# Kernel tuning notes

Measured on AMD Instinct MI355X. Metric: run time of the kernel, lower is better.

## Reference

```python
import jax, jax.numpy as jnp
from jax import lax
import numpy as np

B, T, I, H = 256, 1024, 128, 256


def setup_inputs() -> dict:
    key = jax.random.key(0)
    k1, k2, k3 = jax.random.split(key, 3)
    # Xavier-ish scaling so sigmoid/tanh gates are not saturated
    s_ih = float(np.sqrt(2.0 / (I + 3 * H)))
    s_hh = float(np.sqrt(2.0 / (H + 3 * H)))
    return {
        "x": jax.random.normal(k1, (B, T, I), dtype=jnp.float32),
        "h0": jnp.zeros((B, H), dtype=jnp.float32),
        "weight_ih": jax.random.normal(k2, (3 * H, I), dtype=jnp.float32) * s_ih,
        "weight_hh": jax.random.normal(k3, (3 * H, H), dtype=jnp.float32) * s_hh,
        "bias_ih": jnp.zeros((3 * H,), dtype=jnp.float32),
        "bias_hh": jnp.zeros((3 * H,), dtype=jnp.float32),
    }


def reference(x, h0, weight_ih, weight_hh, bias_ih, bias_hh):
    # Precompute batched input-to-hidden GEMM for all timesteps: [B, T, 3H]
    gates_x = jnp.einsum("bti,gi->btg", x, weight_ih) + bias_ih
    gates_x = jnp.swapaxes(gates_x, 0, 1)  # [T, B, 3H] for scan

    def step(h, gx):
        # NOTE: faithful to source — reset gate multiplies the FULL new-gate
        # preactivation (which already includes the hidden contribution),
        # unlike a standard GRU.
        gates = gx + h @ weight_hh.T + bias_hh  # [B, 3H]
        r, z, n = jnp.split(gates, 3, axis=-1)
        r = jax.nn.sigmoid(r)
        z = jax.nn.sigmoid(z)
        n = jnp.tanh(r * n)
        h_new = (1.0 - z) * h + z * n
        return h_new, h_new

    h_last, outs = lax.scan(step, h0, gates_x)  # outs: [T, B, H]
    output = jnp.swapaxes(outs, 0, 1)  # [B, T, H] (batch_first=True)
    return output, h_last
```

## Files before the change

### kernel.cpp

```cpp
#include <hip/hip_runtime.h>


#define B_SZ 256
#define T_SZ 1024
#define H_SZ 256
#define G3   768
#define NGRP 64
#define SPIN_MAX (1 << 21)
#define HROW 288

typedef __attribute__((ext_vector_type(2))) float f32x2;

template<int CTRL>
__device__ __forceinline__ float dppx(float s) {
    return __int_as_float(
        __builtin_amdgcn_update_dpp(0, __float_as_int(s), CTRL, 0xF, 0xF, true));
}
template<int MASK>
__device__ __forceinline__ float swzx(float s) {
    return __int_as_float(__builtin_amdgcn_ds_swizzle(__float_as_int(s), MASK));
}
__device__ __forceinline__ f32x2 pkfma(f32x2 a, f32x2 b, f32x2 c) {
    f32x2 d;
    asm("v_pk_fma_f32 %0, %1, %2, %3" : "=v"(d) : "v"(a), "v"(b), "v"(c));
    return d;
}

static __device__ __forceinline__ int hpos(int k) { return k + 4 * (k >> 5); }

static __device__ __forceinline__ size_t xsl(int g, int par, int n, int u) {
    return (((size_t)g * 2 + par) * 4 + n) * 256 + u;
}

__global__ void prep_kernel(const float* __restrict__ h0,
                            unsigned long long* __restrict__ xch) {
    int tid = blockIdx.x * blockDim.x + threadIdx.x;
    if (tid < B_SZ * H_SZ) {
        int b = tid >> 8, u = tid & 255;
        int g = b >> 2, n = b & 3;
        unsigned long long val = (unsigned long long)__float_as_uint(h0[tid]);
        xch[xsl(g, 0, n, u)] = val;
        xch[xsl(g, 1, n, u)] = val;
    }
}

__global__ __launch_bounds__(256) void gemm_x_kernel(
    const float* __restrict__ x, const float* __restrict__ wih,
    float* __restrict__ gx, int c, int tcShift)
{
    __shared__ __align__(16) float xs[64][132];
    __shared__ __align__(16) float ws[128][68];
    const int TC = 1 << tcShift;
    const int t  = threadIdx.x;
    const int bx = blockIdx.x, by = blockIdx.y;

#pragma unroll
    for (int i = 0; i < 8; ++i) {
        int f4 = t + i * 256;
        int r  = f4 >> 5, c4 = (f4 & 31) * 4;
        int rho = bx * 64 + r;
        int b = rho >> tcShift, u = rho & (TC - 1);
        float4 v = *(const float4*)(x + ((size_t)b * T_SZ + (size_t)c * TC + u) * 128 + c4);
        *(float4*)&xs[r][c4] = v;
    }

    const int gl = t & 31;
    const int rl = t >> 5;
    float acc[8][4];
#pragma unroll
    for (int i = 0; i < 8; ++i)
#pragma unroll
        for (int jj = 0; jj < 4; ++jj) acc[i][jj] = 0.f;

    for (int kb = 0; kb < 2; ++kb) {
        __syncthreads();
#pragma unroll
        for (int i = 0; i < 8; ++i) {
            int f4 = t + i * 256;
            int row = f4 >> 4, c4 = (f4 & 15) * 4;
            float4 v = *(const float4*)(wih + (size_t)(by * 128 + row) * 128 + kb * 64 + c4);
            *(float4*)&ws[row][c4] = v;
        }
        __syncthreads();

#pragma unroll 4
        for (int k4 = 0; k4 < 16; ++k4) {
            float4 wv0 = *(const float4*)&ws[gl     ][k4 * 4];
            float4 wv1 = *(const float4*)&ws[gl + 32][k4 * 4];
            float4 wv2 = *(const float4*)&ws[gl + 64][k4 * 4];
            float4 wv3 = *(const float4*)&ws[gl + 96][k4 * 4];
#pragma unroll
            for (int rr = 0; rr < 8; ++rr) {
                float4 xv = *(const float4*)&xs[rl + rr * 8][kb * 64 + k4 * 4];
                acc[rr][0] = fmaf(xv.w, wv0.w, fmaf(xv.z, wv0.z, fmaf(xv.y, wv0.y, fmaf(xv.x, wv0.x, acc[rr][0]))));
                acc[rr][1] = fmaf(xv.w, wv1.w, fmaf(xv.z, wv1.z, fmaf(xv.y, wv1.y, fmaf(xv.x, wv1.x, acc[rr][1]))));
                acc[rr][2] = fmaf(xv.w, wv2.w, fmaf(xv.z, wv2.z, fmaf(xv.y, wv2.y, fmaf(xv.x, wv2.x, acc[rr][2]))));
                acc[rr][3] = fmaf(xv.w, wv3.w, fmaf(xv.z, wv3.z, fmaf(xv.y, wv3.y, fmaf(xv.x, wv3.x, acc[rr][3]))));
            }
        }
    }

#pragma unroll
    for (int rr = 0; rr < 8; ++rr) {
        size_t base = (size_t)(bx * 64 + rl + rr * 8) * G3 + by * 128 + gl;
#pragma unroll
        for (int gi = 0; gi < 4; ++gi)
            gx[base + 32 * gi] = acc[rr][gi];
    }
}

#define PIN2(v) asm volatile("" : "+v"(v));

__global__ __launch_bounds__(512)
__attribute__((amdgpu_waves_per_eu(2, 2)))
void gru_kernel(
    const float* __restrict__ gx, const float* __restrict__ whh,
    const float* __restrict__ bih, const float* __restrict__ bhh,
    unsigned long long* __restrict__ xch, float* __restrict__ out,
    int gbase, int tc, int isLast)
{
    __shared__ __align__(16) float hl[2][4][HROW];
    __shared__ __align__(16) float hst[2][4][64];

    const int t   = threadIdx.x;
    const int bid = blockIdx.x;
    const int g   = bid & 63;
    const int m   = bid >> 6;
    const int u0  = m * 64;
    const int q   = t >> 5;
    const int p   = t & 31;
    const int pb  = p & 3;
    const int uq  = u0 + 4 * q;
    const int k0  = 8 * p;

    f32x2 wf[12][4];
#pragma unroll
    for (int gate = 0; gate < 3; ++gate) {
#pragma unroll
        for (int e = 0; e < 4; ++e) {
            const float* wr = whh + (size_t)(gate * 256 + uq + e) * H_SZ + k0;
            float4 va = *(const float4*)(wr);
            float4 vb = *(const float4*)(wr + 4);
            wf[gate * 4 + e][0] = (f32x2){va.x, va.y};
            wf[gate * 4 + e][1] = (f32x2){va.z, va.w};
            wf[gate * 4 + e][2] = (f32x2){vb.x, vb.y};
            wf[gate * 4 + e][3] = (f32x2){vb.z, vb.w};
        }
    }
#pragma unroll
    for (int f = 0; f < 12; ++f) {
        PIN2(wf[f][0]) PIN2(wf[f][1]) PIN2(wf[f][2]) PIN2(wf[f][3])
    }

    const bool act = (p < 16);
    const int  e   = (p >> 2) & 3;
    const int  ue  = uq + e;
    float bsr = 0.f, bsz = 0.f, bsn = 0.f;
    const float* gxp = nullptr;
    if (act) {
        bsr = bih[ue]       + bhh[ue];
        bsz = bih[256 + ue] + bhh[256 + ue];
        bsn = bih[512 + ue] + bhh[512 + ue];
        gxp = gx + ((size_t)(4 * g + pb) * tc) * G3 + ue;
    }

    const int n_t  = t >> 7;
    const int c2   = t & 127;
    const int wofs = 2 * c2 + 4 * (c2 >> 4);
    const int Wd = hpos(k0);
    const int pue = hpos(ue);
    const int n_o = t >> 4, f_o = t & 15;

    float gxr = 0.f, gxz = 0.f, gxn = 0.f;
    if (act) { gxr = gxp[0]; gxz = gxp[256]; gxn = gxp[512]; }

#pragma unroll 1
    for (int u = 0; u < tc; ++u) {
        const int tg   = gbase + u;
        const int par  = tg & 1;
        const int par1 = (tg + 1) & 1;

        {
            unsigned long long* sb = xch + xsl(g, par, n_t, 2 * c2);
            const unsigned want = (unsigned)tg;
            unsigned long long v0, v1;
            int sp = 0;
            for (;;) {
                v0 = __hip_atomic_load(sb + 0, __ATOMIC_RELAXED, __HIP_MEMORY_SCOPE_AGENT);
                v1 = __hip_atomic_load(sb + 1, __ATOMIC_RELAXED, __HIP_MEMORY_SCOPE_AGENT);
                bool ok = ((unsigned)(v0 >> 32) == want) & ((unsigned)(v1 >> 32) == want);
                if (ok || ++sp >= SPIN_MAX) break;
                __builtin_amdgcn_s_sleep(1);
            }
            float2 hv;
            hv.x = __uint_as_float((unsigned)v0);
            hv.y = __uint_as_float((unsigned)v1);
            *(float2*)&hl[par][n_t][wofs] = hv;
        }
        __syncthreads();

        if (u > 0 && t < 64) {
            float4 o;
            o.x = hst[par1][n_o][4 * f_o];     o.y = hst[par1][n_o][4 * f_o + 1];
            o.z = hst[par1][n_o][4 * f_o + 2]; o.w = hst[par1][n_o][4 * f_o + 3];
            *(float4*)(out + ((size_t)(4 * g + n_o) * T_SZ + (tg - 1)) * H_SZ + u0 + 4 * f_o) = o;
        }

        float pgr = 0.f, pgz = 0.f, pgn = 0.f;
        if (act && u + 1 < tc) {
            size_t go = (size_t)(u + 1) * G3;
            pgr = gxp[go]; pgz = gxp[go + 256]; pgn = gxp[go + 512];
        }

        float s[12][4];
        {
            const float* hb = &hl[par][0][0] + Wd;
#pragma unroll
            for (int i = 0; i < 4; ++i) {
                const float* hr = hb + (size_t)(i ^ pb) * HROW;
                float4 hv0 = *(const float4*)(hr);
                float4 hv1 = *(const float4*)(hr + 4);
                f32x2 h0 = (f32x2){hv0.x, hv0.y};
                f32x2 h1 = (f32x2){hv0.z, hv0.w};
                f32x2 h2 = (f32x2){hv1.x, hv1.y};
                f32x2 h3 = (f32x2){hv1.z, hv1.w};
                f32x2 z  = (f32x2){0.f, 0.f};
#pragma unroll
                for (int f = 0; f < 12; ++f) {
                    f32x2 a = pkfma(h0, wf[f][0],
                              pkfma(h1, wf[f][1],
                              pkfma(h2, wf[f][2],
                              pkfma(h3, wf[f][3], z))));
                    s[f][i] = a.x + a.y;
                }
            }
        }

#pragma unroll
        for (int f = 0; f < 12; ++f) {
            s[f][0] += dppx<0xB1>(s[f][1]);
            s[f][2] += dppx<0xB1>(s[f][3]);
            s[f][0] += dppx<0x4E>(s[f][2]);
            s[f][0] += dppx<0x124>(s[f][0]);
            s[f][0] += dppx<0x128>(s[f][0]);
            s[f][0] += swzx<0x401F>(s[f][0]);
        }

        if (act) {
            float sr = (e & 2) ? ((e & 1) ? s[3][0]  : s[2][0])
                               : ((e & 1) ? s[1][0]  : s[0][0]);
            float sz = (e & 2) ? ((e & 1) ? s[7][0]  : s[6][0])
                               : ((e & 1) ? s[5][0]  : s[4][0]);
            float sn = (e & 2) ? ((e & 1) ? s[11][0] : s[10][0])
                               : ((e & 1) ? s[9][0]  : s[8][0]);

            float hold = hl[par][pb][pue];
            float ar = sr + gxr + bsr;
            float az = sz + gxz + bsz;
            float an = sn + gxn + bsn;
            float r  = 1.f / (1.f + expf(-ar));
            float z  = 1.f / (1.f + expf(-az));
            float nn = tanhf(r * an);
            float hn = (1.f - z) * hold + z * nn;

            hst[par][pb][ue - u0] = hn;
            __hip_atomic_store(xch + xsl(g, par1, pb, ue),
                               ((unsigned long long)(unsigned)(tg + 1) << 32) |
                               (unsigned long long)__float_as_uint(hn),
                               __ATOMIC_RELAXED, __HIP_MEMORY_SCOPE_AGENT);
        }
        gxr = pgr; gxz = pgz; gxn = pgn;
    }

    __syncthreads();
    {
        const int fpar = (gbase + tc - 1) & 1;
        if (t < 64) {
            float4 o;
            o.x = hst[fpar][n_o][4 * f_o];     o.y = hst[fpar][n_o][4 * f_o + 1];
            o.z = hst[fpar][n_o][4 * f_o + 2]; o.w = hst[fpar][n_o][4 * f_o + 3];
            *(float4*)(out + ((size_t)(4 * g + n_o) * T_SZ + (gbase + tc - 1)) * H_SZ + u0 + 4 * f_o) = o;
            if (isLast)
                *(float4*)(out + (size_t)B_SZ * T_SZ * H_SZ
                               + (size_t)(4 * g + n_o) * H_SZ + u0 + 4 * f_o) = o;
        }
    }
}

extern "C" void kernel_launch(void* const* d_in, const int* in_sizes, int n_in,
                              void* d_out, int out_size, void* d_ws, size_t ws_size,
                              hipStream_t stream) {
    const float* x   = (const float*)d_in[0];
    const float* h0  = (const float*)d_in[1];
    const float* wih = (const float*)d_in[2];
    const float* whh = (const float*)d_in[3];
    const float* bih = (const float*)d_in[4];
    const float* bhh = (const float*)d_in[5];
    float* out = (float*)d_out;

    char* ws = (char*)d_ws;
    const size_t xchB = (size_t)NGRP * 2 * 4 * 256 * 8;
    unsigned long long* xch = (unsigned long long*)ws;
    float* gxb = (float*)(ws + xchB);

    int tcShift = 10;
    while (tcShift > 0 &&
           xchB + (786432ull << tcShift) > ws_size) --tcShift;
    const int TC  = 1 << tcShift;
    const int nCh = T_SZ / TC;

    prep_kernel<<<dim3(256), dim3(256), 0, stream>>>(h0, xch);
    for (int c = 0; c < nCh; ++c) {
        gemm_x_kernel<<<dim3(B_SZ * TC / 64, 6), dim3(256), 0, stream>>>(
            x, wih, gxb, c, tcShift);
        gru_kernel<<<dim3(B_SZ), dim3(512), 0, stream>>>(
            gxb, whh, bih, bhh, xch, out, c * TC, TC, (c == nCh - 1) ? 1 : 0);
    }
}
```

Baseline: 3.712 ms.

## Repartition GRU blocks to 2 batch rows by 128 hidden units each

Each recurrent block now handles 2 batch rows and 128 hidden units instead of 4 rows and 64 units, so 128 groups cover the batch. Each thread keeps twice as many recurrent weight rows in registers (24 packed rows), and the cross-lane reduction drops one shuffle stage. The intent is to cut the number of rows each block must gather through the global exchange buffer and to shorten the reduction chain per step. In exchange, register pressure roughly doubles for weights, and a second barrier is added per timestep, with hst reused across steps without parity.

Result: slower. 5.913 ms (+59.3%).

```diff
diff --git a/kernel.cpp b/kernel.cpp
--- a/kernel.cpp
+++ b/kernel.cpp
@@ -5,7 +5,7 @@
 #define T_SZ 1024
 #define H_SZ 256
 #define G3   768
-#define NGRP 64
+#define NGRP 128
 #define SPIN_MAX (1 << 21)
 #define HROW 288
 
@@ -29,7 +29,7 @@
 static __device__ __forceinline__ int hpos(int k) { return k + 4 * (k >> 5); }
 
 static __device__ __forceinline__ size_t xsl(int g, int par, int n, int u) {
-    return (((size_t)g * 2 + par) * 4 + n) * 256 + u;
+    return (((size_t)g * 2 + par) * 2 + n) * 256 + u;
 }
 
 __global__ void prep_kernel(const float* __restrict__ h0,
@@ -37,7 +37,7 @@
     int tid = blockIdx.x * blockDim.x + threadIdx.x;
     if (tid < B_SZ * H_SZ) {
         int b = tid >> 8, u = tid & 255;
-        int g = b >> 2, n = b & 3;
+        int g = b >> 1, n = b & 1;
         unsigned long long val = (unsigned long long)__float_as_uint(h0[tid]);
         xch[xsl(g, 0, n, u)] = val;
         xch[xsl(g, 1, n, u)] = val;
@@ -119,92 +119,85 @@
     unsigned long long* __restrict__ xch, float* __restrict__ out,
     int gbase, int tc, int isLast)
 {
-    __shared__ __align__(16) float hl[2][4][HROW];
-    __shared__ __align__(16) float hst[2][4][64];
+    __shared__ __align__(16) float hl[2][HROW];
+    __shared__ __align__(16) float hst[2][128];
 
     const int t   = threadIdx.x;
     const int bid = blockIdx.x;
-    const int g   = bid & 63;
-    const int m   = bid >> 6;
-    const int u0  = m * 64;
+    const int g   = bid & 127;
+    const int m   = bid >> 7;
+    const int u0  = m * 128;
     const int q   = t >> 5;
     const int p   = t & 31;
-    const int pb  = p & 3;
-    const int uq  = u0 + 4 * q;
+    const int pb  = p & 1;
+    const int uo  = u0 + 8 * q;
     const int k0  = 8 * p;
 
-    f32x2 wf[12][4];
+    f32x2 wf[24][4];
 #pragma unroll
     for (int gate = 0; gate < 3; ++gate) {
 #pragma unroll
-        for (int e = 0; e < 4; ++e) {
-            const float* wr = whh + (size_t)(gate * 256 + uq + e) * H_SZ + k0;
+        for (int e = 0; e < 8; ++e) {
+            const float* wr = whh + (size_t)(gate * 256 + uo + e) * H_SZ + k0;
             float4 va = *(const float4*)(wr);
             float4 vb = *(const float4*)(wr + 4);
-            wf[gate * 4 + e][0] = (f32x2){va.x, va.y};
-            wf[gate * 4 + e][1] = (f32x2){va.z, va.w};
-            wf[gate * 4 + e][2] = (f32x2){vb.x, vb.y};
-            wf[gate * 4 + e][3] = (f32x2){vb.z, vb.w};
-        }
-    }
-#pragma unroll
-    for (int f = 0; f < 12; ++f) {
+            wf[gate * 8 + e][0] = (f32x2){va.x, va.y};
+            wf[gate * 8 + e][1] = (f32x2){va.z, va.w};
+            wf[gate * 8 + e][2] = (f32x2){vb.x, vb.y};
+            wf[gate * 8 + e][3] = (f32x2){vb.z, vb.w};
+        }
+    }
+#pragma unroll
+    for (int f = 0; f < 24; ++f) {
         PIN2(wf[f][0]) PIN2(wf[f][1]) PIN2(wf[f][2]) PIN2(wf[f][3])
     }
 
     const bool act = (p < 16);
-    const int  e   = (p >> 2) & 3;
-    const int  ue  = uq + e;
+    const int  e   = p >> 1;
+    const int  ue  = uo + e;
     float bsr = 0.f, bsz = 0.f, bsn = 0.f;
     const float* gxp = nullptr;
     if (act) {
         bsr = bih[ue]       + bhh[ue];
         bsz = bih[256 + ue] + bhh[256 + ue];
         bsn = bih[512 + ue] + bhh[512 + ue];
-        gxp = gx + ((size_t)(4 * g + pb) * tc) * G3 + ue;
-    }
-
-    const int n_t  = t >> 7;
-    const int c2   = t & 127;
-    const int wofs = 2 * c2 + 4 * (c2 >> 4);
-    const int Wd = hpos(k0);
-    const int pue = hpos(ue);
-    const int n_o = t >> 4, f_o = t & 15;
+        gxp = gx + ((size_t)(2 * g + pb) * tc) * G3 + ue;
+    }
+
+    const int n_t  = t >> 8;
+    const int un   = t & 255;
+    const int wofs = hpos(un);
+    const int Wd   = hpos(k0);
+    const int pue  = hpos(ue);
+    const int n_o = t >> 5, f_o = t & 31;
 
     float gxr = 0.f, gxz = 0.f, gxn = 0.f;
     if (act) { gxr = gxp[0]; gxz = gxp[256]; gxn = gxp[512]; }
 
 #pragma unroll 1
     for (int u = 0; u < tc; ++u) {
-        const int tg   = gbase + u;
-        const int par  = tg & 1;
-        const int par1 = (tg + 1) & 1;
-
-        {
-            unsigned long long* sb = xch + xsl(g, par, n_t, 2 * c2);
-            const unsigned want = (unsigned)tg;
-            unsigned long long v0, v1;
-            int sp = 0;
-            for (;;) {
-                v0 = __hip_atomic_load(sb + 0, __ATOMIC_RELAXED, __HIP_MEMORY_SCOPE_AGENT);
-                v1 = __hip_atomic_load(sb + 1, __ATOMIC_RELAXED, __HIP_MEMORY_SCOPE_AGENT);
-                bool ok = ((unsigned)(v0 >> 32) == want) & ((unsigned)(v1 >> 32) == want);
-                if (ok || ++sp >= SPIN_MAX) break;
-                __builtin_amdgcn_s_sleep(1);
-            }
-            float2 hv;
-            hv.x = __uint_as_float((unsigned)v0);
-            hv.y = __uint_as_float((unsigned)v1);
-            *(float2*)&hl[par][n_t][wofs] = hv;
-        }
-        __syncthreads();
+        const int tg  = gbase + u;
+        const int par = tg & 1;
 
         if (u > 0 && t < 64) {
             float4 o;
-            o.x = hst[par1][n_o][4 * f_o];     o.y = hst[par1][n_o][4 * f_o + 1];
-            o.z = hst[par1][n_o][4 * f_o + 2]; o.w = hst[par1][n_o][4 * f_o + 3];
-            *(float4*)(out + ((size_t)(4 * g + n_o) * T_SZ + (tg - 1)) * H_SZ + u0 + 4 * f_o) = o;
-        }
+            o.x = hst[n_o][4 * f_o];     o.y = hst[n_o][4 * f_o + 1];
+            o.z = hst[n_o][4 * f_o + 2]; o.w = hst[n_o][4 * f_o + 3];
+            *(float4*)(out + ((size_t)(2 * g + n_o) * T_SZ + (tg - 1)) * H_SZ + u0 + 4 * f_o) = o;
+        }
+
+        {
+            unsigned long long* sb = xch + xsl(g, par, n_t, un);
+            const unsigned want = (unsigned)tg;
+            unsigned long long v = __hip_atomic_load(sb, __ATOMIC_RELAXED, __HIP_MEMORY_SCOPE_AGENT);
+            int sp = 0;
+            while ((unsigned)(v >> 32) != want && ++sp < SPIN_MAX) {
+                __builtin_amdgcn_s_sleep(1);
+                v = __hip_atomic_load(sb, __ATOMIC_RELAXED, __HIP_MEMORY_SCOPE_AGENT);
+            }
+            hl[n_t][wofs] = __uint_as_float((unsigned)v);
+        }
+        __syncthreads();
 
         float pgr = 0.f, pgz = 0.f, pgn = 0.f;
         if (act && u + 1 < tc) {
@@ -212,49 +205,60 @@
             pgr = gxp[go]; pgz = gxp[go + 256]; pgn = gxp[go + 512];
         }
 
-        float s[12][4];
+        float s[24];
         {
-            const float* hb = &hl[par][0][0] + Wd;
-#pragma unroll
-            for (int i = 0; i < 4; ++i) {
-                const float* hr = hb + (size_t)(i ^ pb) * HROW;
-                float4 hv0 = *(const float4*)(hr);
-                float4 hv1 = *(const float4*)(hr + 4);
-                f32x2 h0 = (f32x2){hv0.x, hv0.y};
-                f32x2 h1 = (f32x2){hv0.z, hv0.w};
-                f32x2 h2 = (f32x2){hv1.x, hv1.y};
-                f32x2 h3 = (f32x2){hv1.z, hv1.w};
-                f32x2 z  = (f32x2){0.f, 0.f};
-#pragma unroll
-                for (int f = 0; f < 12; ++f) {
-                    f32x2 a = pkfma(h0, wf[f][0],
-                              pkfma(h1, wf[f][1],
-                              pkfma(h2, wf[f][2],
-                              pkfma(h3, wf[f][3], z))));
-                    s[f][i] = a.x + a.y;
-                }
+            const float* hrO = &hl[pb][Wd];
+            const float* hrX = &hl[pb ^ 1][Wd];
+            float4 o0 = *(const float4*)(hrO);
+            float4 o1 = *(const float4*)(hrO + 4);
+            float4 x0 = *(const float4*)(hrX);
+            float4 x1 = *(const float4*)(hrX + 4);
+            f32x2 ho0 = (f32x2){o0.x, o0.y}, ho1 = (f32x2){o0.z, o0.w};
+            f32x2 ho2 = (f32x2){o1.x, o1.y}, ho3 = (f32x2){o1.z, o1.w};
+            f32x2 hx0 = (f32x2){x0.x, x0.y}, hx1 = (f32x2){x0.z, x0.w};
+            f32x2 hx2 = (f32x2){x1.x, x1.y}, hx3 = (f32x2){x1.z, x1.w};
+            f32x2 z = (f32x2){0.f, 0.f};
+#pragma unroll
+            for (int f = 0; f < 24; ++f) {
+                f32x2 aO = pkfma(ho0, wf[f][0],
+                           pkfma(ho1, wf[f][1],
+                           pkfma(ho2, wf[f][2],
+                           pkfma(ho3, wf[f][3], z))));
+                f32x2 aX = pkfma(hx0, wf[f][0],
+                           pkfma(hx1, wf[f][1],
+                           pkfma(hx2, wf[f][2],
+                           pkfma(hx3, wf[f][3], z))));
+                float sO = aO.x + aO.y;
+                float sX = aX.x + aX.y;
+                s[f] = sO + dppx<0xB1>(sX);
             }
         }
 
 #pragma unroll
-        for (int f = 0; f < 12; ++f) {
-            s[f][0] += dppx<0xB1>(s[f][1]);
-            s[f][2] += dppx<0xB1>(s[f][3]);
-            s[f][0] += dppx<0x4E>(s[f][2]);
-            s[f][0] += dppx<0x124>(s[f][0]);
-            s[f][0] += dppx<0x128>(s[f][0]);
-            s[f][0] += swzx<0x401F>(s[f][0]);
+        for (int f = 0; f < 24; ++f) {
+            s[f] += dppx<0x4E>(s[f]);
+            s[f] += dppx<0x124>(s[f]);
+            s[f] += dppx<0x128>(s[f]);
+            s[f] += swzx<0x401F>(s[f]);
         }
 
         if (act) {
-            float sr = (e & 2) ? ((e & 1) ? s[3][0]  : s[2][0])
-                               : ((e & 1) ? s[1][0]  : s[0][0]);
-            float sz = (e & 2) ? ((e & 1) ? s[7][0]  : s[6][0])
-                               : ((e & 1) ? s[5][0]  : s[4][0]);
-            float sn = (e & 2) ? ((e & 1) ? s[11][0] : s[10][0])
-                               : ((e & 1) ? s[9][0]  : s[8][0]);
-
-            float hold = hl[par][pb][pue];
+            const bool e0 = (e & 1) != 0, e1 = (e & 2) != 0, e2 = (e & 4) != 0;
+            float r01, r23, r45, r67, ry0, ry1, sr, sz, sn;
+            r01 = e0 ? s[1] : s[0];  r23 = e0 ? s[3] : s[2];
+            r45 = e0 ? s[5] : s[4];  r67 = e0 ? s[7] : s[6];
+            ry0 = e1 ? r23 : r01;    ry1 = e1 ? r67 : r45;
+            sr  = e2 ? ry1 : ry0;
+            r01 = e0 ? s[9]  : s[8];  r23 = e0 ? s[11] : s[10];
+            r45 = e0 ? s[13] : s[12]; r67 = e0 ? s[15] : s[14];
+            ry0 = e1 ? r23 : r01;     ry1 = e1 ? r67 : r45;
+            sz  = e2 ? ry1 : ry0;
+            r01 = e0 ? s[17] : s[16]; r23 = e0 ? s[19] : s[18];
+            r45 = e0 ? s[21] : s[20]; r67 = e0 ? s[23] : s[22];
+            ry0 = e1 ? r23 : r01;     ry1 = e1 ? r67 : r45;
+            sn  = e2 ? ry1 : ry0;
+
+            float hold = hl[pb][pue];
             float ar = sr + gxr + bsr;
             float az = sz + gxz + bsz;
             float an = sn + gxn + bsn;
@@ -263,27 +267,24 @@
             float nn = tanhf(r * an);
             float hn = (1.f - z) * hold + z * nn;
 
-            hst[par][pb][ue - u0] = hn;
-            __hip_atomic_store(xch + xsl(g, par1, pb, ue),
+            hst[pb][ue - u0] = hn;
+            __hip_atomic_store(xch + xsl(g, (tg + 1) & 1, pb, ue),
                                ((unsigned long long)(unsigned)(tg + 1) << 32) |
                                (unsigned long long)__float_as_uint(hn),
                                __ATOMIC_RELAXED, __HIP_MEMORY_SCOPE_AGENT);
         }
         gxr = pgr; gxz = pgz; gxn = pgn;
-    }
-
-    __syncthreads();
-    {
-        const int fpar = (gbase + tc - 1) & 1;
-        if (t < 64) {
-            float4 o;
-            o.x = hst[fpar][n_o][4 * f_o];     o.y = hst[fpar][n_o][4 * f_o + 1];
-            o.z = hst[fpar][n_o][4 * f_o + 2]; o.w = hst[fpar][n_o][4 * f_o + 3];
-            *(float4*)(out + ((size_t)(4 * g + n_o) * T_SZ + (gbase + tc - 1)) * H_SZ + u0 + 4 * f_o) = o;
-            if (isLast)
-                *(float4*)(out + (size_t)B_SZ * T_SZ * H_SZ
-                               + (size_t)(4 * g + n_o) * H_SZ + u0 + 4 * f_o) = o;
-        }
+        __syncthreads();
+    }
+
+    if (t < 64) {
+        float4 o;
+        o.x = hst[n_o][4 * f_o];     o.y = hst[n_o][4 * f_o + 1];
+        o.z = hst[n_o][4 * f_o + 2]; o.w = hst[n_o][4 * f_o + 3];
+        *(float4*)(out + ((size_t)(2 * g + n_o) * T_SZ + (gbase + tc - 1)) * H_SZ + u0 + 4 * f_o) = o;
+        if (isLast)
+            *(float4*)(out + (size_t)B_SZ * T_SZ * H_SZ
+                           + (size_t)(2 * g + n_o) * H_SZ + u0 + 4 * f_o) = o;
     }
 }
 
@@ -299,7 +300,7 @@
     float* out = (float*)d_out;
 
     char* ws = (char*)d_ws;
-    const size_t xchB = (size_t)NGRP * 2 * 4 * 256 * 8;
+    const size_t xchB = (size_t)NGRP * 2 * 2 * 256 * 8;
     unsigned long long* xch = (unsigned long long*)ws;
     float* gxb = (float*)(ws + xchB);
 
```
